# Kernel tuning notes

Hardware: AMD Instinct MI355X
Metric: run time of the kernel (lower is better)

## Reference

```python
import jax, jax.numpy as jnp
import numpy as np

N = 2_000_000
H = 50
N_MID = 7  # number of Linear(50,50)+Tanh blocks


def setup_inputs() -> dict:
    key = jax.random.key(0)
    ks = jax.random.split(key, 9)
    s = 0.1  # small init scale to keep tanh out of saturation
    return {
        "x": jax.random.normal(ks[0], (N, 1), jnp.float32),
        "y": jax.random.normal(ks[1], (N, 1), jnp.float32),
        "z": jax.random.normal(ks[2], (N, 1), jnp.float32),
        "W_in": jax.random.normal(ks[3], (3, H), jnp.float32) * s,
        "b_in": jax.random.normal(ks[4], (H,), jnp.float32) * s,
        "W_mid": jax.random.normal(ks[5], (N_MID, H, H), jnp.float32) * s,
        "b_mid": jax.random.normal(ks[6], (N_MID, H), jnp.float32) * s,
        "W_out": jax.random.normal(ks[7], (H, 3), jnp.float32) * s,
        "b_out": jax.random.normal(ks[8], (3,), jnp.float32) * s,
    }


def reference(x, y, z, W_in, b_in, W_mid, b_mid, W_out, b_out):
    # Uin = hstack(x, y, z) -> [N, 3]
    Uin = jnp.concatenate([x, y, z], axis=1)
    h = jnp.tanh(Uin @ W_in + b_in)            # [N, 50]
    for i in range(N_MID):                      # fixed small layer count
        h = jnp.tanh(h @ W_mid[i] + b_mid[i])   # [N, 50]
    U = h @ W_out + b_out                       # [N, 3]
    return (U[:, 0:1], U[:, 1:2], U[:, 2:3])
```

## Files before the change

### kernel.cpp

```cpp
#include <hip/hip_runtime.h>

#define HID 50
#define NMID 7
#define NT 4
#define NS 2
#define PT 4

#define MID_ELEMS (NMID * NT * NS * 64 * 8)
#define IN_ELEMS  (NT * 64 * 8)
#define OUT_ELEMS (NS * 64 * 8)
#define W_HALFS   (MID_ELEMS + IN_ELEMS + OUT_ELEMS)

#define SCALE 2.8853900817779268f

typedef _Float16 half8  __attribute__((ext_vector_type(8)));
typedef float    f32x4  __attribute__((ext_vector_type(4)));
typedef float    f32x2  __attribute__((ext_vector_type(2)));

__device__ __forceinline__ unsigned short f16hi(float w) {
    _Float16 h = (_Float16)w;
    return __builtin_bit_cast(unsigned short, h);
}
__device__ __forceinline__ unsigned short f16lo(float w) {
    _Float16 h = (_Float16)w;
    _Float16 l = (_Float16)(w - (float)h);
    return __builtin_bit_cast(unsigned short, l);
}

__device__ __forceinline__ int kperm(int k) {
    int s = k >> 5, q = (k >> 3) & 3, j = k & 7;
    return 16 * (2 * s + (j >> 2)) + 4 * q + (j & 3);
}

__device__ __forceinline__ int rowfeat(int rw) {
    if (rw < 48) return rw;
    if (rw == 48) return 48;
    if (rw == 52) return 49;
    return -1;
}

__global__ void pack_params(const float* __restrict__ W_in, const float* __restrict__ b_in,
                            const float* __restrict__ W_mid, const float* __restrict__ b_mid,
                            const float* __restrict__ W_out, const float* __restrict__ b_out,
                            unsigned short* __restrict__ wp) {
    int e = blockIdx.x * 256 + threadIdx.x;
    if (e < MID_ELEMS) {
        int L = e / (NT * NS * 512), r1 = e % (NT * NS * 512);
        int t = r1 / (NS * 512),     r2 = r1 % (NS * 512);
        int s = r2 / 512,            r3 = r2 % 512;
        int l = r3 / 8,              j  = r3 % 8;
        int fo = rowfeat(t * 16 + (l & 15));
        int k  = s * 32 + ((l >> 4) << 3) + j;
        unsigned short bits = 0;
        if (fo >= 0) {
            if (k >= 62) {
                float sum = b_mid[L * HID + fo];
                for (int jj = 0; jj < HID; ++jj) sum += W_mid[(L * HID + jj) * HID + fo];
                float v = SCALE * sum - 1.0f;
                bits = (k == 62) ? f16hi(v) : f16lo(v);
            } else {
                int fi = rowfeat(kperm(k));
                if (fi >= 0) bits = f16hi(-SCALE * W_mid[(L * HID + fi) * HID + fo]);
            }
        }
        wp[e] = bits;
    } else if (e < MID_ELEMS + IN_ELEMS) {
        int e2 = e - MID_ELEMS;
        int t = e2 / 512, r = e2 % 512, l = r / 8, j = r % 8;
        int fo = rowfeat(t * 16 + (l & 15));
        int q  = l >> 4;
        unsigned short bits = 0;
        if (fo >= 0 && q == 0) {
            if (j < 3)       bits = f16hi(SCALE * W_in[j * HID + fo]);
            else if (j < 6)  bits = f16hi(SCALE * W_in[(j - 3) * HID + fo]);
            else {
                float v = SCALE * b_in[fo] - 1.0f;
                bits = (j == 6) ? f16hi(v) : f16lo(v);
            }
        }
        wp[e] = bits;
    } else if (e < W_HALFS) {
        int e3 = e - MID_ELEMS - IN_ELEMS;
        int s = e3 / 512, r = e3 % 512, l = r / 8, j = r % 8;
        int m = l & 15;
        int k = s * 32 + ((l >> 4) << 3) + j;
        unsigned short bits = 0;
        if (m < 3) {
            if (k >= 62) {
                float sum = b_out[m];
                for (int jj = 0; jj < HID; ++jj) sum += W_out[jj * 3 + m];
                bits = (k == 62) ? f16hi(sum) : f16lo(sum);
            } else {
                int fi = rowfeat(kperm(k));
                if (fi >= 0) bits = f16hi(-W_out[fi * 3 + m]);
            }
        }
        wp[e] = bits;
    }
}

__device__ __forceinline__ unsigned int pk2(float a, float b) {
    auto p = __builtin_amdgcn_cvt_pkrtz(a, b);
    return __builtin_bit_cast(unsigned int, p);
}
__device__ __forceinline__ unsigned int rr_pair(float a0, float a1) {
    f32x2 e;
    e[0] = __builtin_amdgcn_exp2f(a0);
    e[1] = __builtin_amdgcn_exp2f(a1);
    f32x2 d = e + 0.5f;
    float inv = __builtin_amdgcn_rcpf(d[0] * d[1]);
    f32x2 r = inv * __builtin_shufflevector(d, d, 1, 0);
    return pk2(r[0], r[1]);
}
__device__ __forceinline__ half8 epi_full(const f32x4& c0, const f32x4& c1) {
    uint4 u;
    u.x = rr_pair(c0[0], c0[1]);
    u.y = rr_pair(c0[2], c0[3]);
    u.z = rr_pair(c1[0], c1[1]);
    u.w = rr_pair(c1[2], c1[3]);
    return __builtin_bit_cast(half8, u);
}
__device__ __forceinline__ half8 epi_tail(const f32x4& c2, const f32x4& c3) {
    uint4 u;
    u.x = rr_pair(c2[0], c2[1]);
    u.y = rr_pair(c2[2], c2[3]);
    float e = __builtin_amdgcn_exp2f(c3[0]);
    float r = __builtin_amdgcn_rcpf(e + 0.5f);
    u.z = pk2(r, 1.0f);
    u.w = 0x3C003C00u;
    return __builtin_bit_cast(half8, u);
}

__global__ __launch_bounds__(256, 4) void softmesh_mfma(
    const float* __restrict__ x, const float* __restrict__ y,
    const float* __restrict__ z,
    const unsigned short* __restrict__ wp,
    float* __restrict__ out, int n)
{
    const int tid  = threadIdx.x;
    const int wave = tid >> 6, lane = tid & 63;
    const int m = lane & 15, quad = lane >> 4;

    const int i0 = (blockIdx.x * 4 + wave) * 64;
    if (i0 >= n) return;

    const half8* __restrict__ Wm = (const half8*)wp;
    const half8* __restrict__ Wi = Wm + MID_ELEMS / 8;
    const half8* __restrict__ Wo = Wi + IN_ELEMS / 8;

    half8 Ain[NT];
#pragma unroll
    for (int t = 0; t < NT; ++t) Ain[t] = Wi[t * 64 + lane];
    half8 A[NT * NS];
#pragma unroll
    for (int i = 0; i < NT * NS; ++i) A[i] = Wm[i * 64 + lane];

    half8 B[PT][NS];

#pragma unroll
    for (int pt = 0; pt < PT; ++pt) {
        int idx = min(i0 + pt * 16 + m, n - 1);
        half8 bf = {0, 0, 0, 0, 0, 0, 0, 0};
        if (quad == 0) {
            float xv = x[idx], yv = y[idx], zv = z[idx];
            _Float16 xh = (_Float16)xv, yh = (_Float16)yv, zh = (_Float16)zv;
            bf[0] = xh; bf[1] = yh; bf[2] = zh;
            bf[3] = (_Float16)(xv - (float)xh);
            bf[4] = (_Float16)(yv - (float)yh);
            bf[5] = (_Float16)(zv - (float)zh);
            bf[6] = (_Float16)1.0f; bf[7] = (_Float16)1.0f;
        }
        f32x4 cc[NT];
#pragma unroll
        for (int t = 0; t < NT; ++t) {
            f32x4 z4 = (f32x4){0.f, 0.f, 0.f, 0.f};
            cc[t] = __builtin_amdgcn_mfma_f32_16x16x32_f16(Ain[t], bf, z4, 0, 0, 0);
        }
        B[pt][0] = epi_full(cc[0], cc[1]);
        B[pt][1] = epi_tail(cc[2], cc[3]);
    }

#pragma unroll
    for (int L = 0; L < NMID; ++L) {
        half8 An[NT * NS];
        if (L < NMID - 1) {
#pragma unroll
            for (int i = 0; i < NT * NS; ++i) An[i] = Wm[((L + 1) * NT * NS + i) * 64 + lane];
        } else {
            An[0] = Wo[lane]; An[1] = Wo[64 + lane];
#pragma unroll
            for (int i = 2; i < NT * NS; ++i) An[i] = A[i];
        }
#pragma unroll
        for (int pt = 0; pt < PT; ++pt) {
            f32x4 cc[NT];
#pragma unroll
            for (int t = 0; t < NT; ++t) {
                f32x4 z4 = (f32x4){0.f, 0.f, 0.f, 0.f};
                f32x4 c = __builtin_amdgcn_mfma_f32_16x16x32_f16(A[t * NS + 0], B[pt][0], z4, 0, 0, 0);
                cc[t]   = __builtin_amdgcn_mfma_f32_16x16x32_f16(A[t * NS + 1], B[pt][1], c,  0, 0, 0);
            }
            B[pt][0] = epi_full(cc[0], cc[1]);
            B[pt][1] = epi_tail(cc[2], cc[3]);
        }
#pragma unroll
        for (int i = 0; i < NT * NS; ++i) A[i] = An[i];
    }

#pragma unroll
    for (int pt = 0; pt < PT; ++pt) {
        f32x4 z4 = (f32x4){0.f, 0.f, 0.f, 0.f};
        f32x4 c = __builtin_amdgcn_mfma_f32_16x16x32_f16(A[0], B[pt][0], z4, 0, 0, 0);
        c       = __builtin_amdgcn_mfma_f32_16x16x32_f16(A[1], B[pt][1], c,  0, 0, 0);
        if (quad == 0) {
            int idx = i0 + pt * 16 + m;
            if (idx < n) {
                out[idx] = c[0];
                out[(size_t)n + idx] = c[1];
                out[2 * (size_t)n + idx] = c[2];
            }
        }
    }
}

extern "C" void kernel_launch(void* const* d_in, const int* in_sizes, int n_in,
                              void* d_out, int out_size, void* d_ws, size_t ws_size,
                              hipStream_t stream) {
    const float* x     = (const float*)d_in[0];
    const float* y     = (const float*)d_in[1];
    const float* z     = (const float*)d_in[2];
    const float* W_in  = (const float*)d_in[3];
    const float* b_in  = (const float*)d_in[4];
    const float* W_mid = (const float*)d_in[5];
    const float* b_mid = (const float*)d_in[6];
    const float* W_out = (const float*)d_in[7];
    const float* b_out = (const float*)d_in[8];
    float* out = (float*)d_out;
    int n = in_sizes[0];

    unsigned short* wpp = (unsigned short*)d_ws;

    int pgrid = (W_HALFS + 255) / 256;
    pack_params<<<pgrid, 256, 0, stream>>>(W_in, b_in, W_mid, b_mid, W_out, b_out, wpp);

    int grid = (n + 255) / 256;
    softmesh_mfma<<<grid, 256, 0, stream>>>(x, y, z, wpp, out, n);
}
```

Before: 264.6 us.

## Software-pipeline MFMA and tanh epilogue across point tiles, share reciprocals

```diff
diff --git a/kernel.cpp b/kernel.cpp
--- a/kernel.cpp
+++ b/kernel.cpp
@@ -103,32 +103,49 @@
     auto p = __builtin_amdgcn_cvt_pkrtz(a, b);
     return __builtin_bit_cast(unsigned int, p);
 }
-__device__ __forceinline__ unsigned int rr_pair(float a0, float a1) {
-    f32x2 e;
-    e[0] = __builtin_amdgcn_exp2f(a0);
-    e[1] = __builtin_amdgcn_exp2f(a1);
-    f32x2 d = e + 0.5f;
-    float inv = __builtin_amdgcn_rcpf(d[0] * d[1]);
-    f32x2 r = inv * __builtin_shufflevector(d, d, 1, 0);
-    return pk2(r[0], r[1]);
+__device__ __forceinline__ void rr_quad(float a0, float a1, float a2, float a3,
+                                        unsigned int& u0, unsigned int& u1) {
+    f32x2 e01, e23;
+    e01[0] = __builtin_amdgcn_exp2f(a0);
+    e01[1] = __builtin_amdgcn_exp2f(a1);
+    e23[0] = __builtin_amdgcn_exp2f(a2);
+    e23[1] = __builtin_amdgcn_exp2f(a3);
+    f32x2 d01 = e01 + 0.5f;
+    f32x2 d23 = e23 + 0.5f;
+    float p01 = d01[0] * d01[1];
+    float p23 = d23[0] * d23[1];
+    float inv = __builtin_amdgcn_rcpf(p01 * p23);
+    f32x2 i01 = {inv * p23, inv * p23};
+    f32x2 i23 = {inv * p01, inv * p01};
+    f32x2 r01 = i01 * __builtin_shufflevector(d01, d01, 1, 0);
+    f32x2 r23 = i23 * __builtin_shufflevector(d23, d23, 1, 0);
+    u0 = pk2(r01[0], r01[1]);
+    u1 = pk2(r23[0], r23[1]);
 }
 __device__ __forceinline__ half8 epi_full(const f32x4& c0, const f32x4& c1) {
     uint4 u;
-    u.x = rr_pair(c0[0], c0[1]);
-    u.y = rr_pair(c0[2], c0[3]);
-    u.z = rr_pair(c1[0], c1[1]);
-    u.w = rr_pair(c1[2], c1[3]);
+    rr_quad(c0[0], c0[1], c0[2], c0[3], u.x, u.y);
+    rr_quad(c1[0], c1[1], c1[2], c1[3], u.z, u.w);
     return __builtin_bit_cast(half8, u);
 }
 __device__ __forceinline__ half8 epi_tail(const f32x4& c2, const f32x4& c3) {
     uint4 u;
-    u.x = rr_pair(c2[0], c2[1]);
-    u.y = rr_pair(c2[2], c2[3]);
+    rr_quad(c2[0], c2[1], c2[2], c2[3], u.x, u.y);
     float e = __builtin_amdgcn_exp2f(c3[0]);
     float r = __builtin_amdgcn_rcpf(e + 0.5f);
     u.z = pk2(r, 1.0f);
     u.w = 0x3C003C00u;
     return __builtin_bit_cast(half8, u);
+}
+
+__device__ __forceinline__ void mfma_mid(const half8 (&A)[NT * NS], const half8 (&Bp)[NS],
+                                         f32x4 (&cc)[NT]) {
+#pragma unroll
+    for (int t = 0; t < NT; ++t) {
+        f32x4 z4 = (f32x4){0.f, 0.f, 0.f, 0.f};
+        f32x4 c = __builtin_amdgcn_mfma_f32_16x16x32_f16(A[t * NS + 0], Bp[0], z4, 0, 0, 0);
+        cc[t]   = __builtin_amdgcn_mfma_f32_16x16x32_f16(A[t * NS + 1], Bp[1], c,  0, 0, 0);
+    }
 }
 
 __global__ __launch_bounds__(256, 4) void softmesh_mfma(
@@ -144,6 +161,13 @@
     const int i0 = (blockIdx.x * 4 + wave) * 64;
     if (i0 >= n) return;
 
+    float xv[PT], yv[PT], zv[PT];
+#pragma unroll
+    for (int pt = 0; pt < PT; ++pt) {
+        int idx = min(i0 + pt * 16 + m, n - 1);
+        if (quad == 0) { xv[pt] = x[idx]; yv[pt] = y[idx]; zv[pt] = z[idx]; }
+    }
+
     const half8* __restrict__ Wm = (const half8*)wp;
     const half8* __restrict__ Wi = Wm + MID_ELEMS / 8;
     const half8* __restrict__ Wo = Wi + IN_ELEMS / 8;
@@ -156,53 +180,78 @@
     for (int i = 0; i < NT * NS; ++i) A[i] = Wm[i * 64 + lane];
 
     half8 B[PT][NS];
-
-#pragma unroll
-    for (int pt = 0; pt < PT; ++pt) {
-        int idx = min(i0 + pt * 16 + m, n - 1);
-        half8 bf = {0, 0, 0, 0, 0, 0, 0, 0};
-        if (quad == 0) {
-            float xv = x[idx], yv = y[idx], zv = z[idx];
-            _Float16 xh = (_Float16)xv, yh = (_Float16)yv, zh = (_Float16)zv;
-            bf[0] = xh; bf[1] = yh; bf[2] = zh;
-            bf[3] = (_Float16)(xv - (float)xh);
-            bf[4] = (_Float16)(yv - (float)yh);
-            bf[5] = (_Float16)(zv - (float)zh);
-            bf[6] = (_Float16)1.0f; bf[7] = (_Float16)1.0f;
-        }
-        f32x4 cc[NT];
-#pragma unroll
-        for (int t = 0; t < NT; ++t) {
-            f32x4 z4 = (f32x4){0.f, 0.f, 0.f, 0.f};
-            cc[t] = __builtin_amdgcn_mfma_f32_16x16x32_f16(Ain[t], bf, z4, 0, 0, 0);
-        }
-        B[pt][0] = epi_full(cc[0], cc[1]);
-        B[pt][1] = epi_tail(cc[2], cc[3]);
+    f32x4 cc0[NT], cc1[NT];
+
+    {
+        half8 bf[PT];
+#pragma unroll
+        for (int pt = 0; pt < PT; ++pt) {
+            half8 b8 = {0, 0, 0, 0, 0, 0, 0, 0};
+            if (quad == 0) {
+                _Float16 xh = (_Float16)xv[pt], yh = (_Float16)yv[pt], zh = (_Float16)zv[pt];
+                b8[0] = xh; b8[1] = yh; b8[2] = zh;
+                b8[3] = (_Float16)(xv[pt] - (float)xh);
+                b8[4] = (_Float16)(yv[pt] - (float)yh);
+                b8[5] = (_Float16)(zv[pt] - (float)zh);
+                b8[6] = (_Float16)1.0f; b8[7] = (_Float16)1.0f;
+            }
+            bf[pt] = b8;
+        }
+#pragma unroll
+        for (int t = 0; t < NT; ++t) {
+            f32x4 z4 = (f32x4){0.f, 0.f, 0.f, 0.f};
+            cc0[t] = __builtin_amdgcn_mfma_f32_16x16x32_f16(Ain[t], bf[0], z4, 0, 0, 0);
+        }
+#pragma unroll
+        for (int t = 0; t < NT; ++t) {
+            f32x4 z4 = (f32x4){0.f, 0.f, 0.f, 0.f};
+            cc1[t] = __builtin_amdgcn_mfma_f32_16x16x32_f16(Ain[t], bf[1], z4, 0, 0, 0);
+        }
+        B[0][0] = epi_full(cc0[0], cc0[1]); B[0][1] = epi_tail(cc0[2], cc0[3]);
+#pragma unroll
+        for (int t = 0; t < NT; ++t) {
+            f32x4 z4 = (f32x4){0.f, 0.f, 0.f, 0.f};
+            cc0[t] = __builtin_amdgcn_mfma_f32_16x16x32_f16(Ain[t], bf[2], z4, 0, 0, 0);
+        }
+        B[1][0] = epi_full(cc1[0], cc1[1]); B[1][1] = epi_tail(cc1[2], cc1[3]);
+#pragma unroll
+        for (int t = 0; t < NT; ++t) {
+            f32x4 z4 = (f32x4){0.f, 0.f, 0.f, 0.f};
+            cc1[t] = __builtin_amdgcn_mfma_f32_16x16x32_f16(Ain[t], bf[3], z4, 0, 0, 0);
+        }
+        B[2][0] = epi_full(cc0[0], cc0[1]); B[2][1] = epi_tail(cc0[2], cc0[3]);
+        B[3][0] = epi_full(cc1[0], cc1[1]); B[3][1] = epi_tail(cc1[2], cc1[3]);
     }
 
 #pragma unroll
     for (int L = 0; L < NMID; ++L) {
+        const bool last = (L == NMID - 1);
         half8 An[NT * NS];
-        if (L < NMID - 1) {
-#pragma unroll
-            for (int i = 0; i < NT * NS; ++i) An[i] = Wm[((L + 1) * NT * NS + i) * 64 + lane];
-        } else {
-            An[0] = Wo[lane]; An[1] = Wo[64 + lane];
-#pragma unroll
-            for (int i = 2; i < NT * NS; ++i) An[i] = A[i];
-        }
-#pragma unroll
-        for (int pt = 0; pt < PT; ++pt) {
-            f32x4 cc[NT];
-#pragma unroll
-            for (int t = 0; t < NT; ++t) {
-                f32x4 z4 = (f32x4){0.f, 0.f, 0.f, 0.f};
-                f32x4 c = __builtin_amdgcn_mfma_f32_16x16x32_f16(A[t * NS + 0], B[pt][0], z4, 0, 0, 0);
-                cc[t]   = __builtin_amdgcn_mfma_f32_16x16x32_f16(A[t * NS + 1], B[pt][1], c,  0, 0, 0);
-            }
-            B[pt][0] = epi_full(cc[0], cc[1]);
-            B[pt][1] = epi_tail(cc[2], cc[3]);
-        }
+
+        mfma_mid(A, B[0], cc0);
+        if (!last) { An[0] = Wm[((L + 1) * 8 + 0) * 64 + lane];
+                     An[1] = Wm[((L + 1) * 8 + 1) * 64 + lane]; }
+        else       { An[0] = Wo[lane]; An[1] = Wo[64 + lane]; }
+
+        mfma_mid(A, B[1], cc1);
+        if (!last) { An[2] = Wm[((L + 1) * 8 + 2) * 64 + lane];
+                     An[3] = Wm[((L + 1) * 8 + 3) * 64 + lane]; }
+        else       { An[2] = A[2]; An[3] = A[3]; }
+        B[0][0] = epi_full(cc0[0], cc0[1]); B[0][1] = epi_tail(cc0[2], cc0[3]);
+
+        mfma_mid(A, B[2], cc0);
+        if (!last) { An[4] = Wm[((L + 1) * 8 + 4) * 64 + lane];
+                     An[5] = Wm[((L + 1) * 8 + 5) * 64 + lane]; }
+        else       { An[4] = A[4]; An[5] = A[5]; }
+        B[1][0] = epi_full(cc1[0], cc1[1]); B[1][1] = epi_tail(cc1[2], cc1[3]);
+
+        mfma_mid(A, B[3], cc1);
+        if (!last) { An[6] = Wm[((L + 1) * 8 + 6) * 64 + lane];
+                     An[7] = Wm[((L + 1) * 8 + 7) * 64 + lane]; }
+        else       { An[6] = A[6]; An[7] = A[7]; }
+        B[2][0] = epi_full(cc0[0], cc0[1]); B[2][1] = epi_tail(cc0[2], cc0[3]);
+
+        B[3][0] = epi_full(cc1[0], cc1[1]); B[3][1] = epi_tail(cc1[2], cc1[3]);
 #pragma unroll
         for (int i = 0; i < NT * NS; ++i) A[i] = An[i];
     }
```

Result: slower. 272.5 us (+3.0%).
